# Kernel optimization log

Hardware: AMD Instinct MI355X
Metric: run time of the kernel (lower is better)

## Reference

```python
import jax, jax.numpy as jnp
import numpy as np

N = 100000      # nodes
E = 1600000     # edges
F_IN = 512      # num_features
HEADS = 8
C1 = 8          # per-head channels, layer 1
NCLS = 40       # num_classes
NEG_SLOPE = 0.2


def setup_inputs() -> dict:
    key = jax.random.key(0)
    ks = jax.random.split(key, 10)
    x = jax.random.normal(ks[0], (N, F_IN), jnp.float32)
    edge_index = jax.random.randint(ks[1], (2, E), 0, N, dtype=jnp.int64)
    s1 = 1.0 / np.sqrt(F_IN)
    s2 = 1.0 / np.sqrt(HEADS * C1)
    W1 = jax.random.normal(ks[2], (F_IN, HEADS * C1), jnp.float32) * s1
    att_src1 = jax.random.normal(ks[3], (HEADS, C1), jnp.float32) * s2
    att_dst1 = jax.random.normal(ks[4], (HEADS, C1), jnp.float32) * s2
    b1 = jnp.zeros((HEADS * C1,), jnp.float32)
    W2 = jax.random.normal(ks[5], (HEADS * C1, NCLS), jnp.float32) * s2
    att_src2 = jax.random.normal(ks[6], (1, NCLS), jnp.float32) * 0.1
    att_dst2 = jax.random.normal(ks[7], (1, NCLS), jnp.float32) * 0.1
    b2 = jnp.zeros((NCLS,), jnp.float32)
    return {"x": x, "edge_index": edge_index,
            "W1": W1, "att_src1": att_src1, "att_dst1": att_dst1, "b1": b1,
            "W2": W2, "att_src2": att_src2, "att_dst2": att_dst2, "b2": b2}


def gat_conv(x, src, dst, W, att_src, att_dst, b, heads, cout):
    """PyG-style GATConv (eval mode: dropout off). src->dst message flow."""
    n = x.shape[0]
    h = (x @ W).reshape(n, heads, cout)                 # [N, H, C]
    a_s = jnp.sum(h * att_src, axis=-1)                 # [N, H]
    a_d = jnp.sum(h * att_dst, axis=-1)                 # [N, H]
    e = jax.nn.leaky_relu(a_s[src] + a_d[dst], NEG_SLOPE)  # [Etot, H]
    # segment softmax over incoming edges of each dst node
    m = jax.lax.stop_gradient(jax.ops.segment_max(e, dst, num_segments=n))
    ex = jnp.exp(e - m[dst])
    den = jax.ops.segment_sum(ex, dst, num_segments=n)
    alpha = ex / (den[dst] + 1e-16)                     # [Etot, H]
    msg = h[src] * alpha[..., None]                     # [Etot, H, C]
    out = jax.ops.segment_sum(msg, dst, num_segments=n) # [N, H, C]
    return out.reshape(n, heads * cout) + b


def reference(x, edge_index, W1, att_src1, att_dst1, b1, W2, att_src2, att_dst2, b2):
    n = x.shape[0]
    loops = jnp.arange(n, dtype=edge_index.dtype)       # GATConv add_self_loops=True
    src = jnp.concatenate([edge_index[0], loops])
    dst = jnp.concatenate([edge_index[1], loops])
    h = jax.nn.elu(gat_conv(x, src, dst, W1, att_src1, att_dst1, b1, HEADS, C1))
    out = gat_conv(h, src, dst, W2, att_src2, att_dst2, b2, 1, NCLS)
    return jax.nn.log_softmax(out, axis=1)
```

## Files before the change

kernel.cpp:

```cpp
#include <hip/hip_runtime.h>
#include <hip/hip_bf16.h>
#include <math.h>

#define F_IN 512
#define HOUT 64
#define HEADS 8
#define C1 8
#define NCLS 40
#define NEG 0.2f

#define DPB 256
#define CAP 8064
#define EPT 32
#define WLD 520

typedef __attribute__((ext_vector_type(8))) short short8;
typedef __attribute__((ext_vector_type(4))) float f32x4;

__device__ __forceinline__ ushort f2b(float f) {
    union { float f; unsigned u; } v; v.f = f;
    unsigned r = (v.u + 0x7FFFu + ((v.u >> 16) & 1u)) >> 16;
    return (ushort)r;
}
__device__ __forceinline__ float b2f(ushort b) {
    union { unsigned u; float f; } v; v.u = ((unsigned)b) << 16;
    return v.f;
}
__device__ __forceinline__ float b2f_lo(unsigned u) { union { unsigned u; float f; } v; v.u = u << 16; return v.f; }
__device__ __forceinline__ float b2f_hi(unsigned u) { union { unsigned u; float f; } v; v.u = u & 0xFFFF0000u; return v.f; }


__global__ __launch_bounds__(256) void prep_k(const float* __restrict__ W1, const float* __restrict__ W2,
                                              int* __restrict__ gcur, ushort* __restrict__ Wtg,
                                              ushort* __restrict__ W2t, int nbuck) {
    int bid = blockIdx.x, t = threadIdx.x;
    if (bid < 128) {
        int idx = bid * 256 + t;
        int k = idx >> 6, c = idx & 63;
        Wtg[(size_t)c * WLD + k] = f2b(W1[idx]);
    } else if (bid < 140) {
        int idx = (bid - 128) * 256 + t;
        int c = idx >> 6, k = idx & 63;
        W2t[idx] = (c < NCLS) ? f2b(W2[k * NCLS + c]) : 0;
    } else {
        int b = (bid - 140) * 256 + t;
        if (b < nbuck) gcur[b] = b * CAP;
    }
}


__device__ void gemm1_body(int bid, const float* __restrict__ x, const ushort* __restrict__ Wtg,
                           ushort* __restrict__ h1b, int n, ushort Asd[128][40]) {
    int tid = threadIdx.x;
    int lane = tid & 63, wid = tid >> 6;
    int lr = lane & 15, lg = lane >> 4;
    int row0 = bid * 128;
    f32x4 acc[2][4];
#pragma unroll
    for (int rt = 0; rt < 2; ++rt)
#pragma unroll
        for (int ct = 0; ct < 4; ++ct) acc[rt][ct] = (f32x4){0.f, 0.f, 0.f, 0.f};

    for (int k0 = 0; k0 < F_IN; k0 += 32) {
#pragma unroll
        for (int j = 0; j < 4; ++j) {
            int idx = tid + j * 256;
            int r = idx >> 3;
            int k4 = (idx & 7) << 2;
            int gr = row0 + r;
            float4 v = (gr < n) ? *(const float4*)&x[(size_t)gr * F_IN + k0 + k4]
                                : make_float4(0.f, 0.f, 0.f, 0.f);
            ushort4 b4 = make_ushort4(f2b(v.x), f2b(v.y), f2b(v.z), f2b(v.w));
            *(ushort4*)&Asd[r][k4] = b4;
        }
        __syncthreads();
        short8 af[2], bf[4];
#pragma unroll
        for (int rt = 0; rt < 2; ++rt)
            af[rt] = *(const short8*)&Asd[wid * 32 + rt * 16 + lr][lg * 8];
#pragma unroll
        for (int ct = 0; ct < 4; ++ct)
            bf[ct] = *(const short8*)&Wtg[(size_t)(ct * 16 + lr) * WLD + k0 + lg * 8];
#pragma unroll
        for (int rt = 0; rt < 2; ++rt)
#pragma unroll
            for (int ct = 0; ct < 4; ++ct)
                acc[rt][ct] = __builtin_amdgcn_mfma_f32_16x16x32_bf16(af[rt], bf[ct], acc[rt][ct], 0, 0, 0);
        __syncthreads();
    }
#pragma unroll
    for (int rt = 0; rt < 2; ++rt)
#pragma unroll
        for (int q = 0; q < 4; ++q) {
            int gr = row0 + wid * 32 + rt * 16 + lg * 4 + q;
            if (gr < n) {
#pragma unroll
                for (int ct = 0; ct < 4; ++ct)
                    h1b[(size_t)gr * HOUT + ct * 16 + lr] = f2b(acc[rt][ct][q]);
            }
        }
}

__device__ void passA_body(int bid, const int* __restrict__ ei, int* __restrict__ gcur,
                           int* __restrict__ bkt, int E, int Etot, int nbuck,
                           int* hist, int* lbase) {
    int t = threadIdx.x;
    int base_e = bid * (256 * EPT);
    for (int j = t; j < 512; j += 256) hist[j] = 0;
    __syncthreads();
    for (int j = 0; j < EPT; ++j) {
        int idx = base_e + j * 256 + t;
        if (idx < Etot) {
            int d = (idx < E) ? ei[E + idx] : (idx - E);
            atomicAdd(&hist[d >> 8], 1);
        }
    }
    __syncthreads();
    for (int j = t; j < nbuck; j += 256) {
        int c = hist[j];
        lbase[j] = c ? atomicAdd(&gcur[j], c) : 0;
    }
    __syncthreads();
    for (int j = t; j < 512; j += 256) hist[j] = 0;
    __syncthreads();
    for (int j = 0; j < EPT; ++j) {
        int idx = base_e + j * 256 + t;
        if (idx < Etot) {
            int s, d;
            if (idx < E) { s = ei[idx]; d = ei[E + idx]; } else { s = idx - E; d = idx - E; }
            int b = d >> 8;
            int slot = atomicAdd(&hist[b], 1);
            bkt[lbase[b] + slot] = (s << 8) | (d & 255);
        }
    }
}

__global__ __launch_bounds__(256) void work1_k(const float* __restrict__ x, const ushort* __restrict__ Wtg,
                                               ushort* __restrict__ h1b, int n,
                                               const int* __restrict__ ei, int* __restrict__ gcur,
                                               int* __restrict__ bkt, int E, int Etot, int nbuck, int g1) {
    __shared__ ushort Asd[128][40];
    __shared__ int hist[512];
    __shared__ int lbase[512];
    if ((int)blockIdx.x < g1) gemm1_body(blockIdx.x, x, Wtg, h1b, n, Asd);
    else passA_body(blockIdx.x - g1, ei, gcur, bkt, E, Etot, nbuck, hist, lbase);
}


__device__ void passB_body(int b, const int* __restrict__ bkt, const int* __restrict__ gcur,
                           int2* __restrict__ rowse, int* __restrict__ col, int n,
                           int* hist, int* lcur, int* wsum) {
    int t = threadIdx.x;
    int cnt = gcur[b] - b * CAP;
    int base = b * CAP;
    int d0 = b * DPB;
    int ndst = min(DPB, n - d0);
    const int* src = bkt + (size_t)b * CAP;
    hist[t] = 0;
    __syncthreads();
    for (int e = t; e < cnt; e += 256) {
        atomicAdd(&hist[src[e] & 255], 1);
    }
    __syncthreads();
    int v = hist[t];
    int lane = t & 63, w = t >> 6;
    int ss = v;
#pragma unroll
    for (int off = 1; off < 64; off <<= 1) { int t2 = __shfl_up(ss, off); if (lane >= off) ss += t2; }
    if (lane == 63) wsum[w] = ss;
    __syncthreads();
    int woff = 0;
    for (int j = 0; j < w; ++j) woff += wsum[j];
    int excl = woff + ss - v;
    if (t < ndst) rowse[d0 + t] = make_int2(base + excl, base + excl + v);
    lcur[t] = excl;
    __syncthreads();
    for (int e = t; e < cnt; e += 256) {
        int u = src[e];
        int pos = atomicAdd(&lcur[u & 255], 1);
        col[base + pos] = (int)((unsigned)u >> 8);
    }
}

__device__ void att1_body(int bid, const ushort* __restrict__ h1b, const float* __restrict__ asw,
                          const float* __restrict__ adw, float* __restrict__ as1,
                          float* __restrict__ ad1, int n) {
    int t = bid * 256 + threadIdx.x;
    if (t >= n * HEADS) return;
    int hd = t & 7;
    const ushort* hp = h1b + (size_t)(t >> 3) * HOUT + hd * C1;
    short8 hv = *(const short8*)hp;
    float4 a0 = *(const float4*)(asw + hd * C1), a1 = *(const float4*)(asw + hd * C1 + 4);
    float4 d0 = *(const float4*)(adw + hd * C1), d1 = *(const float4*)(adw + hd * C1 + 4);
    float h0 = b2f((ushort)hv[0]), h1 = b2f((ushort)hv[1]), h2 = b2f((ushort)hv[2]), h3 = b2f((ushort)hv[3]);
    float h4 = b2f((ushort)hv[4]), h5 = b2f((ushort)hv[5]), h6 = b2f((ushort)hv[6]), h7 = b2f((ushort)hv[7]);
    as1[t] = h0*a0.x + h1*a0.y + h2*a0.z + h3*a0.w + h4*a1.x + h5*a1.y + h6*a1.z + h7*a1.w;
    ad1[t] = h0*d0.x + h1*d0.y + h2*d0.z + h3*d0.w + h4*d1.x + h5*d1.y + h6*d1.z + h7*d1.w;
}

__global__ __launch_bounds__(256) void work2_k(const int* __restrict__ bkt, const int* __restrict__ gcur,
                                               int2* __restrict__ rowse, int* __restrict__ col, int n,
                                               const ushort* __restrict__ h1b, const float* __restrict__ asw,
                                               const float* __restrict__ adw, float* __restrict__ as1,
                                               float* __restrict__ ad1, int gpb) {
    __shared__ int hist[DPB];
    __shared__ int lcur[DPB];
    __shared__ int wsum[4];
    if ((int)blockIdx.x < gpb) passB_body(blockIdx.x, bkt, gcur, rowse, col, n, hist, lcur, wsum);
    else att1_body(blockIdx.x - gpb, h1b, asw, adw, as1, ad1, n);
}


__global__ __launch_bounds__(256) void l1agg_k(const ushort* __restrict__ h1b, const float* __restrict__ as1,
                                               const float* __restrict__ ad1, const float* __restrict__ b1,
                                               const int2* __restrict__ rowse, const int* __restrict__ col,
                                               ushort* __restrict__ hactb, int n) {
    __shared__ int2 pk_all[4][2 * 273];
    int wid = threadIdx.x >> 6, lane = threadIdx.x & 63;
    int nA = (blockIdx.x * 4 + wid) * 2;
    if (nA >= n) return;
    int nB = nA + 1;
    int na = lane >> 5, sl = lane & 31;
    int node = nA + na;
    bool nodev = node < n;
    int4 rr = *(const int4*)&rowse[nA];
    if (nB >= n) { rr.z = rr.y; rr.w = rr.y; }
    int degA = rr.y - rr.x, degB = rr.w - rr.z;
    int st  = na ? rr.z : rr.x;
    int deg = na ? degB : degA;
    int2* pk = pk_all[wid];

    if (degA <= 32 && degB <= 32) {
        bool v = nodev && (sl < deg);
        int s = 0;
        float4 a0 = make_float4(0.f, 0.f, 0.f, 0.f), a1 = a0;
        if (v) {
            s = col[st + sl];
            a0 = *(const float4*)&as1[s * 8];
            a1 = *(const float4*)&as1[s * 8 + 4];
        }
        float4 d0 = make_float4(0.f, 0.f, 0.f, 0.f), d1 = d0;
        if (nodev) {
            d0 = *(const float4*)&ad1[node * 8];
            d1 = *(const float4*)&ad1[node * 8 + 4];
        }
        float ea[8] = {a0.x + d0.x, a0.y + d0.y, a0.z + d0.z, a0.w + d0.w,
                       a1.x + d1.x, a1.y + d1.y, a1.z + d1.z, a1.w + d1.w};
#pragma unroll
        for (int h = 0; h < 8; ++h) {
            float e0 = ea[h];
            float ee = v ? (e0 >= 0.f ? e0 : NEG * e0) : -1e30f;
            pk[na * 273 + h * 34 + sl] = make_int2(__float_as_int(ee), s);
        }
        __asm__ volatile("s_waitcnt lgkmcnt(0)" ::: "memory");
        __builtin_amdgcn_sched_barrier(0);
        {
            int t = lane & 3, h = (lane >> 2) & 7, na2 = lane >> 5;
            int base = na2 * 273 + h * 34;
            float e[8];
#pragma unroll
            for (int u = 0; u < 8; ++u) e[u] = __int_as_float(pk[base + t + 4 * u].x);
            float mx = e[0];
#pragma unroll
            for (int u = 1; u < 8; ++u) mx = fmaxf(mx, e[u]);
            mx = fmaxf(mx, __shfl_xor(mx, 1));
            mx = fmaxf(mx, __shfl_xor(mx, 2));
            float p[8], sm = 0.f;
#pragma unroll
            for (int u = 0; u < 8; ++u) { p[u] = __expf(e[u] - mx); sm += p[u]; }
            sm += __shfl_xor(sm, 1);
            sm += __shfl_xor(sm, 2);
            float inv = 1.f / (sm + 1e-16f);
#pragma unroll
            for (int u = 0; u < 8; ++u) pk[base + t + 4 * u].x = __float_as_int(p[u] * inv);
        }
        __asm__ volatile("s_waitcnt lgkmcnt(0)" ::: "memory");
        __builtin_amdgcn_sched_barrier(0);
        int cl = sl & 15;
        int eo = sl >> 4;
        int pb = na * 273 + (cl >> 1) * 34 + eo;
        float acc0 = 0.f, acc1 = 0.f, acc2 = 0.f, acc3 = 0.f;
        int mdeg = max(degA, degB);
        for (int g0 = 0; 2 * g0 < mdeg; g0 += 4) {
            int2 qa = pk[pb + 2 * g0];
            int2 qb = pk[pb + 2 * g0 + 2];
            int2 qc = pk[pb + 2 * g0 + 4];
            int2 qd = pk[pb + 2 * g0 + 6];
            uint2 ha = *(const uint2*)&h1b[(size_t)qa.y * HOUT + 4 * cl];
            uint2 hb = *(const uint2*)&h1b[(size_t)qb.y * HOUT + 4 * cl];
            uint2 hc = *(const uint2*)&h1b[(size_t)qc.y * HOUT + 4 * cl];
            uint2 hd = *(const uint2*)&h1b[(size_t)qd.y * HOUT + 4 * cl];
            float wa = __int_as_float(qa.x), wb = __int_as_float(qb.x);
            float wc = __int_as_float(qc.x), wd = __int_as_float(qd.x);
            acc0 += wa * b2f_lo(ha.x) + wb * b2f_lo(hb.x) + wc * b2f_lo(hc.x) + wd * b2f_lo(hd.x);
            acc1 += wa * b2f_hi(ha.x) + wb * b2f_hi(hb.x) + wc * b2f_hi(hc.x) + wd * b2f_hi(hd.x);
            acc2 += wa * b2f_lo(ha.y) + wb * b2f_lo(hb.y) + wc * b2f_lo(hc.y) + wd * b2f_lo(hd.y);
            acc3 += wa * b2f_hi(ha.y) + wb * b2f_hi(hb.y) + wc * b2f_hi(hc.y) + wd * b2f_hi(hd.y);
        }
        acc0 += __shfl_xor(acc0, 16);
        acc1 += __shfl_xor(acc1, 16);
        acc2 += __shfl_xor(acc2, 16);
        acc3 += __shfl_xor(acc3, 16);
        if (nodev && eo == 0) {
            float4 bb = *(const float4*)&b1[4 * cl];
            float o0 = acc0 + bb.x, o1 = acc1 + bb.y, o2 = acc2 + bb.z, o3 = acc3 + bb.w;
            float e0 = o0 > 0.f ? o0 : expm1f(o0);
            float e1 = o1 > 0.f ? o1 : expm1f(o1);
            float e2 = o2 > 0.f ? o2 : expm1f(o2);
            float e3 = o3 > 0.f ? o3 : expm1f(o3);
            ushort4 op = make_ushort4(f2b(e0), f2b(e1), f2b(e2), f2b(e3));
            *(ushort4*)&hactb[(size_t)node * HOUT + 4 * cl] = op;
        }
    } else {
        int hd = sl >> 2;
        float ad = nodev ? ad1[node * 8 + hd] : 0.f;
        float m = -1e30f, den = 0.f, a0 = 0.f, a1 = 0.f;
        int en = st + deg;
        for (int e = st; e < en; ++e) {
            int s = col[e];
            float e0 = as1[s * 8 + hd] + ad;
            float ee = e0 >= 0.f ? e0 : NEG * e0;
            unsigned hv = *(const unsigned*)&h1b[(size_t)s * HOUT + 2 * sl];
            float mn = fmaxf(m, ee);
            float sc = __expf(m - mn), p = __expf(ee - mn);
            den = den * sc + p;
            a0 = a0 * sc + p * b2f_lo(hv);
            a1 = a1 * sc + p * b2f_hi(hv);
            m = mn;
        }
        float2 bb = *(const float2*)&b1[2 * sl];
        float o0 = a0 / (den + 1e-16f) + bb.x;
        float o1 = a1 / (den + 1e-16f) + bb.y;
        float e0 = o0 > 0.f ? o0 : expm1f(o0);
        float e1 = o1 > 0.f ? o1 : expm1f(o1);
        unsigned op = (unsigned)f2b(e0) | ((unsigned)f2b(e1) << 16);
        if (nodev) *(unsigned*)&hactb[(size_t)node * HOUT + 2 * sl] = op;
    }
}


__global__ __launch_bounds__(256) void g2_k(const ushort* __restrict__ hactb, const ushort* __restrict__ W2t,
                                            const float* __restrict__ asw, const float* __restrict__ adw,
                                            ushort* __restrict__ h2b, float* __restrict__ as2,
                                            float* __restrict__ ad2, int n) {
    int tid = threadIdx.x;
    int lane = tid & 63, wid = tid >> 6;
    int lr = lane & 15, lg = lane >> 4;
    int row0 = blockIdx.x * 64 + wid * 16;
    if (row0 >= n) return;
    int gr = row0 + lr;
    bool vr = gr < n;
    f32x4 acc[3];
#pragma unroll
    for (int ct = 0; ct < 3; ++ct) acc[ct] = (f32x4){0.f, 0.f, 0.f, 0.f};
    const short8 z8 = (short8){0, 0, 0, 0, 0, 0, 0, 0};
#pragma unroll
    for (int ks = 0; ks < 2; ++ks) {
        short8 af = vr ? *(const short8*)&hactb[(size_t)gr * HOUT + ks * 32 + lg * 8] : z8;
#pragma unroll
        for (int ct = 0; ct < 3; ++ct) {
            short8 bf = *(const short8*)&W2t[(ct * 16 + lr) * HOUT + ks * 32 + lg * 8];
            acc[ct] = __builtin_amdgcn_mfma_f32_16x16x32_bf16(af, bf, acc[ct], 0, 0, 0);
        }
    }
    float av4[4], dv4[4];
#pragma unroll
    for (int q = 0; q < 4; ++q) {
        int r = row0 + lg * 4 + q;
        bool vw = r < n;
        float av = 0.f, dv = 0.f;
#pragma unroll
        for (int ct = 0; ct < 3; ++ct) {
            int c = ct * 16 + lr;
            if (c < NCLS) {
                float o = acc[ct][q];
                av += o * asw[c];
                dv += o * adw[c];
                if (vw) h2b[(size_t)r * NCLS + c] = f2b(o);
            }
        }
        av += __shfl_xor(av, 1); av += __shfl_xor(av, 2); av += __shfl_xor(av, 4); av += __shfl_xor(av, 8);
        dv += __shfl_xor(dv, 1); dv += __shfl_xor(dv, 2); dv += __shfl_xor(dv, 4); dv += __shfl_xor(dv, 8);
        av4[q] = av; dv4[q] = dv;
    }
#pragma unroll
    for (int q = 0; q < 4; ++q) {
        int r = row0 + lg * 4 + q;
        if (lr == q && r < n) as2[r] = av4[q];
        if (lr == 8 + q && r < n) ad2[r] = dv4[q];
    }
}


__global__ __launch_bounds__(256) void l2agg_k(const ushort* __restrict__ h2b, const float* __restrict__ as2,
                                               const float* __restrict__ ad2, const float* __restrict__ b2,
                                               const int2* __restrict__ rowse, const int* __restrict__ col,
                                               float* __restrict__ out, int n) {
    __shared__ int2 pk_all[4][2 * 40];
    int wid = threadIdx.x >> 6, lane = threadIdx.x & 63;
    int nA = (blockIdx.x * 4 + wid) * 2;
    if (nA >= n) return;
    int nB = nA + 1;
    int na = lane >> 5, sl = lane & 31;
    int node = nA + na;
    bool nodev = node < n;
    int4 rr = *(const int4*)&rowse[nA];
    if (nB >= n) { rr.z = rr.y; rr.w = rr.y; }
    int degA = rr.y - rr.x, degB = rr.w - rr.z;
    int st  = na ? rr.z : rr.x;
    int deg = na ? degB : degA;

    if (degA <= 32 && degB <= 32) {
        int2* pk = pk_all[wid];
        bool v = nodev && (sl < deg);
        int s = 0; float av = 0.f;
        if (v) { s = col[st + sl]; av = as2[s]; }
        float ad = nodev ? ad2[node] : 0.f;
        float ev = av + ad;
        float ee = v ? (ev >= 0.f ? ev : NEG * ev) : -1e30f;
        float m = ee;
        m = fmaxf(m, __shfl_xor(m, 1)); m = fmaxf(m, __shfl_xor(m, 2));
        m = fmaxf(m, __shfl_xor(m, 4)); m = fmaxf(m, __shfl_xor(m, 8));
        m = fmaxf(m, __shfl_xor(m, 16));
        float p = __expf(ee - m);
        float d = p;
        d += __shfl_xor(d, 1); d += __shfl_xor(d, 2); d += __shfl_xor(d, 4);
        d += __shfl_xor(d, 8); d += __shfl_xor(d, 16);
        float w = p / (d + 1e-16f);
        pk[na * 40 + sl] = make_int2(__float_as_int(w), s);
        __asm__ volatile("s_waitcnt lgkmcnt(0)" ::: "memory");
        __builtin_amdgcn_sched_barrier(0);
        bool gact = sl < 20;
        int cl = sl % 10;
        int eo2 = gact ? (sl / 10) : 0;
        int jb = na * 40 + eo2;
        float acc0 = 0.f, acc1 = 0.f, acc2 = 0.f, acc3 = 0.f;
        int mdeg = max(degA, degB);
        for (int g0 = 0; 2 * g0 < mdeg; g0 += 4) {
            int2 qa = pk[jb + 2 * g0];
            int2 qb = pk[jb + 2 * g0 + 2];
            int2 qc = pk[jb + 2 * g0 + 4];
            int2 qd = pk[jb + 2 * g0 + 6];
            if (gact) {
                uint2 ha = *(const uint2*)&h2b[(size_t)qa.y * NCLS + 4 * cl];
                uint2 hb = *(const uint2*)&h2b[(size_t)qb.y * NCLS + 4 * cl];
                uint2 hc = *(const uint2*)&h2b[(size_t)qc.y * NCLS + 4 * cl];
                uint2 hd = *(const uint2*)&h2b[(size_t)qd.y * NCLS + 4 * cl];
                float wa = __int_as_float(qa.x), wb = __int_as_float(qb.x);
                float wc = __int_as_float(qc.x), wd = __int_as_float(qd.x);
                acc0 += wa * b2f_lo(ha.x) + wb * b2f_lo(hb.x) + wc * b2f_lo(hc.x) + wd * b2f_lo(hd.x);
                acc1 += wa * b2f_hi(ha.x) + wb * b2f_hi(hb.x) + wc * b2f_hi(hc.x) + wd * b2f_hi(hd.x);
                acc2 += wa * b2f_lo(ha.y) + wb * b2f_lo(hb.y) + wc * b2f_lo(hc.y) + wd * b2f_lo(hd.y);
                acc3 += wa * b2f_hi(ha.y) + wb * b2f_hi(hb.y) + wc * b2f_hi(hc.y) + wd * b2f_hi(hd.y);
            }
        }
        int self = threadIdx.x & 63;
        float p0 = __shfl(acc0, self + 10);
        float p1 = __shfl(acc1, self + 10);
        float p2s = __shfl(acc2, self + 10);
        float p3 = __shfl(acc3, self + 10);
        bool fin = sl < 10;
        float z0, z1, z2, z3;
        if (fin) {
            float4 bb = *(const float4*)&b2[4 * cl];
            z0 = acc0 + p0 + bb.x; z1 = acc1 + p1 + bb.y;
            z2 = acc2 + p2s + bb.z; z3 = acc3 + p3 + bb.w;
        } else { z0 = z1 = z2 = z3 = -1e30f; }
        float zm = fin ? fmaxf(fmaxf(z0, z1), fmaxf(z2, z3)) : -1e30f;
        zm = fmaxf(zm, __shfl_xor(zm, 1)); zm = fmaxf(zm, __shfl_xor(zm, 2));
        zm = fmaxf(zm, __shfl_xor(zm, 4)); zm = fmaxf(zm, __shfl_xor(zm, 8));
        float ex = fin ? (__expf(z0 - zm) + __expf(z1 - zm) + __expf(z2 - zm) + __expf(z3 - zm)) : 0.f;
        ex += __shfl_xor(ex, 1); ex += __shfl_xor(ex, 2);
        ex += __shfl_xor(ex, 4); ex += __shfl_xor(ex, 8);
        float ls = logf(ex);
        if (fin && nodev) {
            float4 o = make_float4(z0 - zm - ls, z1 - zm - ls, z2 - zm - ls, z3 - zm - ls);
            *(float4*)&out[(size_t)node * NCLS + 4 * cl] = o;
        }
    } else {
        bool act = sl < 20;
        float z0, z1;
        float ad = nodev ? ad2[node] : 0.f;
        float m = -1e30f, den = 0.f, a0 = 0.f, a1 = 0.f;
        int en = st + deg;
        for (int e = st; e < en; ++e) {
            int s = col[e];
            float ev = as2[s] + ad;
            float ee = ev >= 0.f ? ev : NEG * ev;
            float mn = fmaxf(m, ee);
            float sc = __expf(m - mn), p = __expf(ee - mn);
            den = den * sc + p;
            if (act) {
                unsigned hv = *(const unsigned*)&h2b[(size_t)s * NCLS + 2 * sl];
                a0 = a0 * sc + p * b2f_lo(hv);
                a1 = a1 * sc + p * b2f_hi(hv);
            }
            m = mn;
        }
        if (act) {
            float2 bb = *(const float2*)&b2[2 * sl];
            z0 = a0 / (den + 1e-16f) + bb.x;
            z1 = a1 / (den + 1e-16f) + bb.y;
        } else { z0 = z1 = -1e30f; }
        float zm = fmaxf(z0, z1);
        zm = fmaxf(zm, __shfl_xor(zm, 1)); zm = fmaxf(zm, __shfl_xor(zm, 2));
        zm = fmaxf(zm, __shfl_xor(zm, 4)); zm = fmaxf(zm, __shfl_xor(zm, 8));
        zm = fmaxf(zm, __shfl_xor(zm, 16));
        float ex = act ? (__expf(z0 - zm) + __expf(z1 - zm)) : 0.f;
        ex += __shfl_xor(ex, 1); ex += __shfl_xor(ex, 2); ex += __shfl_xor(ex, 4);
        ex += __shfl_xor(ex, 8); ex += __shfl_xor(ex, 16);
        float ls = logf(ex);
        if (act && nodev) {
            float2 o = make_float2(z0 - zm - ls, z1 - zm - ls);
            *(float2*)&out[(size_t)node * NCLS + 2 * sl] = o;
        }
    }
}


extern "C" void kernel_launch(void* const* d_in, const int* in_sizes, int n_in,
                              void* d_out, int out_size, void* d_ws, size_t ws_size,
                              hipStream_t stream) {
    const float* x    = (const float*)d_in[0];
    const int*   ei   = (const int*)d_in[1];
    const float* W1   = (const float*)d_in[2];
    const float* asw1 = (const float*)d_in[3];
    const float* adw1 = (const float*)d_in[4];
    const float* b1   = (const float*)d_in[5];
    const float* W2   = (const float*)d_in[6];
    const float* asw2 = (const float*)d_in[7];
    const float* adw2 = (const float*)d_in[8];
    const float* b2   = (const float*)d_in[9];
    float* out = (float*)d_out;

    const int n = in_sizes[0] / F_IN;
    const int E = in_sizes[1] / 2;
    const int Etot = E + n;
    const int nbuck = (n + DPB - 1) / DPB;
    const int npair = (n + 1) / 2;

    char* ws = (char*)d_ws;
    size_t off = 0;
    auto alloc = [&](size_t bytes) -> void* {
        void* p = ws + off;
        off = (off + bytes + 255) & ~(size_t)255;
        return p;
    };
    int*    gcur   = (int*)alloc((size_t)nbuck * 4);
    int2*   rowse  = (int2*)alloc((size_t)(n + 2) * 8);
    int*    col    = (int*)alloc((size_t)nbuck * CAP * 4);
    int*    bkt    = (int*)alloc((size_t)nbuck * CAP * 4);
    ushort* h1b    = (ushort*)alloc((size_t)n * HOUT * 2);
    float*  as1    = (float*)alloc((size_t)n * HEADS * 4);
    float*  ad1    = (float*)alloc((size_t)n * HEADS * 4);
    ushort* hactb  = (ushort*)alloc((size_t)n * HOUT * 2);
    ushort* Wtg    = (ushort*)alloc((size_t)HOUT * WLD * 2);
    ushort* W2t    = (ushort*)alloc((size_t)48 * HOUT * 2);
    ushort* h2b = h1b;
    float*  as2 = (float*)(h1b + (size_t)n * NCLS);
    float*  ad2 = as2 + n;

    const int g1 = (n + 127) / 128;
    const int gpa = (Etot + 256 * EPT - 1) / (256 * EPT);
    const int gpb = nbuck;
    const int gat = (n * HEADS + 255) / 256;

    prep_k<<<142, 256, 0, stream>>>(W1, W2, gcur, Wtg, W2t, nbuck);
    work1_k<<<g1 + gpa, 256, 0, stream>>>(x, Wtg, h1b, n, ei, gcur, bkt, E, Etot, nbuck, g1);
    work2_k<<<gpb + gat, 256, 0, stream>>>(bkt, gcur, rowse, col, n,
                                           h1b, asw1, adw1, as1, ad1, gpb);
    l1agg_k<<<(npair + 3) / 4, 256, 0, stream>>>(h1b, as1, ad1, b1, rowse, col, hactb, n);
    g2_k<<<(n + 63) / 64, 256, 0, stream>>>(hactb, W2t, asw2, adw2, h2b, as2, ad2, n);
    l2agg_k<<<(npair + 3) / 4, 256, 0, stream>>>(h2b, as2, ad2, b2, rowse, col, out, n);
}
```

Before: 218.1 us.

## Fuse layer-1 aggregation with layer-2 projection through LDS

Merges the layer-1 aggregation kernel and the layer-2 GEMM kernel. Each 512-thread block aggregates 16 nodes, writes the ELU-activated bf16 rows into a swizzled LDS tile, then one wavefront runs the MFMA projection and attention dot products. This removes the global round trip of the hidden activations and one kernel launch. In exchange, seven of eight waves sit idle during the GEMM tail, the block size doubles, and LDS use grows. h2b now gets its own buffer instead of aliasing h1b, since h1b is still being read during the fused kernel.

```diff
diff --git a/kernel.cpp b/kernel.cpp
--- a/kernel.cpp
+++ b/kernel.cpp
@@ -211,19 +211,23 @@
 }
 
 
-__global__ __launch_bounds__(256) void l1agg_k(const ushort* __restrict__ h1b, const float* __restrict__ as1,
-                                               const float* __restrict__ ad1, const float* __restrict__ b1,
-                                               const int2* __restrict__ rowse, const int* __restrict__ col,
-                                               ushort* __restrict__ hactb, int n) {
-    __shared__ int2 pk_all[4][2 * 273];
+__global__ __launch_bounds__(512) void l1g2_k(const ushort* __restrict__ h1b, const float* __restrict__ as1,
+                                              const float* __restrict__ ad1, const float* __restrict__ b1,
+                                              const int2* __restrict__ rowse, const int* __restrict__ col,
+                                              const ushort* __restrict__ W2t, const float* __restrict__ asw,
+                                              const float* __restrict__ adw, ushort* __restrict__ h2b,
+                                              float* __restrict__ as2, float* __restrict__ ad2, int n) {
+    __shared__ int2 pk_all[8][2 * 273];
+    __shared__ ushort hact_lds[16 * 64];
     int wid = threadIdx.x >> 6, lane = threadIdx.x & 63;
-    int nA = (blockIdx.x * 4 + wid) * 2;
-    if (nA >= n) return;
+    int nA = (blockIdx.x * 8 + wid) * 2;
     int nB = nA + 1;
     int na = lane >> 5, sl = lane & 31;
     int node = nA + na;
     bool nodev = node < n;
-    int4 rr = *(const int4*)&rowse[nA];
+    int nd = wid * 2 + na;
+    int4 rr = make_int4(0, 0, 0, 0);
+    if (nA < n) rr = *(const int4*)&rowse[nA];
     if (nB >= n) { rr.z = rr.y; rr.w = rr.y; }
     int degA = rr.y - rr.x, degB = rr.w - rr.z;
     int st  = na ? rr.z : rr.x;
@@ -301,7 +305,7 @@
         acc1 += __shfl_xor(acc1, 16);
         acc2 += __shfl_xor(acc2, 16);
         acc3 += __shfl_xor(acc3, 16);
-        if (nodev && eo == 0) {
+        if (eo == 0) {
             float4 bb = *(const float4*)&b1[4 * cl];
             float o0 = acc0 + bb.x, o1 = acc1 + bb.y, o2 = acc2 + bb.z, o3 = acc3 + bb.w;
             float e0 = o0 > 0.f ? o0 : expm1f(o0);
@@ -309,7 +313,8 @@
             float e2 = o2 > 0.f ? o2 : expm1f(o2);
             float e3 = o3 > 0.f ? o3 : expm1f(o3);
             ushort4 op = make_ushort4(f2b(e0), f2b(e1), f2b(e2), f2b(e3));
-            *(ushort4*)&hactb[(size_t)node * HOUT + 4 * cl] = op;
+            int byte = nd * 128 + ((8 * cl) ^ ((nd & 7) << 4));
+            *(ushort4*)((char*)hact_lds + byte) = op;
         }
     } else {
         int hd = sl >> 2;
@@ -334,60 +339,53 @@
         float e0 = o0 > 0.f ? o0 : expm1f(o0);
         float e1 = o1 > 0.f ? o1 : expm1f(o1);
         unsigned op = (unsigned)f2b(e0) | ((unsigned)f2b(e1) << 16);
-        if (nodev) *(unsigned*)&hactb[(size_t)node * HOUT + 2 * sl] = op;
-    }
-}
-
-
-__global__ __launch_bounds__(256) void g2_k(const ushort* __restrict__ hactb, const ushort* __restrict__ W2t,
-                                            const float* __restrict__ asw, const float* __restrict__ adw,
-                                            ushort* __restrict__ h2b, float* __restrict__ as2,
-                                            float* __restrict__ ad2, int n) {
-    int tid = threadIdx.x;
-    int lane = tid & 63, wid = tid >> 6;
-    int lr = lane & 15, lg = lane >> 4;
-    int row0 = blockIdx.x * 64 + wid * 16;
-    if (row0 >= n) return;
-    int gr = row0 + lr;
-    bool vr = gr < n;
-    f32x4 acc[3];
-#pragma unroll
-    for (int ct = 0; ct < 3; ++ct) acc[ct] = (f32x4){0.f, 0.f, 0.f, 0.f};
-    const short8 z8 = (short8){0, 0, 0, 0, 0, 0, 0, 0};
-#pragma unroll
-    for (int ks = 0; ks < 2; ++ks) {
-        short8 af = vr ? *(const short8*)&hactb[(size_t)gr * HOUT + ks * 32 + lg * 8] : z8;
-#pragma unroll
-        for (int ct = 0; ct < 3; ++ct) {
-            short8 bf = *(const short8*)&W2t[(ct * 16 + lr) * HOUT + ks * 32 + lg * 8];
-            acc[ct] = __builtin_amdgcn_mfma_f32_16x16x32_bf16(af, bf, acc[ct], 0, 0, 0);
-        }
-    }
-    float av4[4], dv4[4];
-#pragma unroll
-    for (int q = 0; q < 4; ++q) {
-        int r = row0 + lg * 4 + q;
-        bool vw = r < n;
-        float av = 0.f, dv = 0.f;
-#pragma unroll
-        for (int ct = 0; ct < 3; ++ct) {
-            int c = ct * 16 + lr;
-            if (c < NCLS) {
-                float o = acc[ct][q];
-                av += o * asw[c];
-                dv += o * adw[c];
-                if (vw) h2b[(size_t)r * NCLS + c] = f2b(o);
+        int byte = nd * 128 + ((4 * sl) ^ ((nd & 7) << 4));
+        *(unsigned*)((char*)hact_lds + byte) = op;
+    }
+
+    __syncthreads();
+    if (wid == 0) {
+        int lr = lane & 15, lg = lane >> 4;
+        int row0 = blockIdx.x * 16;
+        f32x4 acc[3];
+#pragma unroll
+        for (int ct = 0; ct < 3; ++ct) acc[ct] = (f32x4){0.f, 0.f, 0.f, 0.f};
+#pragma unroll
+        for (int ks = 0; ks < 2; ++ks) {
+            int byte = lr * 128 + ((ks * 64 + lg * 16) ^ ((lr & 7) << 4));
+            short8 af = *(const short8*)((char*)hact_lds + byte);
+#pragma unroll
+            for (int ct = 0; ct < 3; ++ct) {
+                short8 bf = *(const short8*)&W2t[(ct * 16 + lr) * HOUT + ks * 32 + lg * 8];
+                acc[ct] = __builtin_amdgcn_mfma_f32_16x16x32_bf16(af, bf, acc[ct], 0, 0, 0);
             }
         }
-        av += __shfl_xor(av, 1); av += __shfl_xor(av, 2); av += __shfl_xor(av, 4); av += __shfl_xor(av, 8);
-        dv += __shfl_xor(dv, 1); dv += __shfl_xor(dv, 2); dv += __shfl_xor(dv, 4); dv += __shfl_xor(dv, 8);
-        av4[q] = av; dv4[q] = dv;
-    }
-#pragma unroll
-    for (int q = 0; q < 4; ++q) {
-        int r = row0 + lg * 4 + q;
-        if (lr == q && r < n) as2[r] = av4[q];
-        if (lr == 8 + q && r < n) ad2[r] = dv4[q];
+        float av4[4], dv4[4];
+#pragma unroll
+        for (int q = 0; q < 4; ++q) {
+            int r = row0 + lg * 4 + q;
+            bool vw = r < n;
+            float av = 0.f, dv = 0.f;
+#pragma unroll
+            for (int ct = 0; ct < 3; ++ct) {
+                int c = ct * 16 + lr;
+                if (c < NCLS) {
+                    float o = acc[ct][q];
+                    av += o * asw[c];
+                    dv += o * adw[c];
+                    if (vw) h2b[(size_t)r * NCLS + c] = f2b(o);
+                }
+            }
+            av += __shfl_xor(av, 1); av += __shfl_xor(av, 2); av += __shfl_xor(av, 4); av += __shfl_xor(av, 8);
+            dv += __shfl_xor(dv, 1); dv += __shfl_xor(dv, 2); dv += __shfl_xor(dv, 4); dv += __shfl_xor(dv, 8);
+            av4[q] = av; dv4[q] = dv;
+        }
+#pragma unroll
+        for (int q = 0; q < 4; ++q) {
+            int r = row0 + lg * 4 + q;
+            if (lr == q && r < n) as2[r] = av4[q];
+            if (lr == 8 + q && r < n) ad2[r] = dv4[q];
+        }
     }
 }
 
@@ -553,23 +551,23 @@
     ushort* h1b    = (ushort*)alloc((size_t)n * HOUT * 2);
     float*  as1    = (float*)alloc((size_t)n * HEADS * 4);
     float*  ad1    = (float*)alloc((size_t)n * HEADS * 4);
-    ushort* hactb  = (ushort*)alloc((size_t)n * HOUT * 2);
+    ushort* h2b    = (ushort*)alloc((size_t)n * NCLS * 2);
+    float*  as2    = (float*)alloc((size_t)n * 4);
+    float*  ad2    = (float*)alloc((size_t)n * 4);
     ushort* Wtg    = (ushort*)alloc((size_t)HOUT * WLD * 2);
     ushort* W2t    = (ushort*)alloc((size_t)48 * HOUT * 2);
-    ushort* h2b = h1b;
-    float*  as2 = (float*)(h1b + (size_t)n * NCLS);
-    float*  ad2 = as2 + n;
 
     const int g1 = (n + 127) / 128;
     const int gpa = (Etot + 256 * EPT - 1) / (256 * EPT);
     const int gpb = nbuck;
     const int gat = (n * HEADS + 255) / 256;
+    const int g16 = (n + 15) / 16;
 
     prep_k<<<142, 256, 0, stream>>>(W1, W2, gcur, Wtg, W2t, nbuck);
     work1_k<<<g1 + gpa, 256, 0, stream>>>(x, Wtg, h1b, n, ei, gcur, bkt, E, Etot, nbuck, g1);
     work2_k<<<gpb + gat, 256, 0, stream>>>(bkt, gcur, rowse, col, n,
                                            h1b, asw1, adw1, as1, ad1, gpb);
-    l1agg_k<<<(npair + 3) / 4, 256, 0, stream>>>(h1b, as1, ad1, b1, rowse, col, hactb, n);
-    g2_k<<<(n + 63) / 64, 256, 0, stream>>>(hactb, W2t, asw2, adw2, h2b, as2, ad2, n);
+    l1g2_k<<<g16, 512, 0, stream>>>(h1b, as1, ad1, b1, rowse, col,
+                                    W2t, asw2, adw2, h2b, as2, ad2, n);
     l2agg_k<<<(npair + 3) / 4, 256, 0, stream>>>(h2b, as2, ad2, b2, rowse, col, out, n);
 }
```

Result: no change. 219.0 us (+0.4%).
